# Optimization experiments

Measured on AMD Instinct MI355X. Metric: run time of the kernel, lower is better.

Reference implementation:

```python
import jax, jax.numpy as jnp
import numpy as np

C_DIM, Q_NUM, U_NUM, BATCH = 512, 8000, 20000, 128


def _edges(key, src_lo, src_hi, dst_lo, dst_hi, n_edges):
    k1, k2 = jax.random.split(key)
    src = jax.random.randint(k1, (n_edges,), src_lo, src_hi, dtype=jnp.int32)
    dst = jax.random.randint(k2, (n_edges,), dst_lo, dst_hi, dtype=jnp.int32)
    return jnp.stack([src, dst])


def setup_inputs() -> dict:
    key = jax.random.key(0)
    ks = jax.random.split(key, 20)
    C, Q, U, B = C_DIM, Q_NUM, U_NUM, BATCH
    inv = 1.0 / np.sqrt(C)
    q_tab = (jax.random.uniform(ks[0], (Q, C)) < (4.0 / C)).astype(jnp.float32)
    q_tab = q_tab.at[:, 0].set(1.0)  # ensure every question has >=1 concept
    return {
        'user_id': jax.random.randint(ks[1], (B,), 0, U, dtype=jnp.int32),
        'question_id': jax.random.randint(ks[2], (B,), 0, Q, dtype=jnp.int32),
        'q_table': q_tab,
        'edges_dir': _edges(ks[3], 0, C, 0, C, 4096),
        'edges_und': _edges(ks[4], 0, C, 0, C, 8192),
        'edges_ke': _edges(ks[5], 0, Q, Q, Q + C, 40000),   # exercise -> concept
        'edges_ek': _edges(ks[6], Q, Q + C, 0, Q, 40000),   # concept -> exercise
        'edges_ue': _edges(ks[7], 0, Q, Q, Q + U, 100000),  # exercise -> student
        'edges_eu': _edges(ks[8], Q, Q + U, 0, Q, 100000),  # student -> exercise
        'user_emb': jax.random.normal(ks[9], (U, C)) * inv,
        'question_emb': jax.random.normal(ks[10], (Q, C)) * inv,
        'concept_emb': jax.random.normal(ks[11], (C, C)) * inv,
        'gat_W': jax.random.normal(ks[12], (2, 6, C, C)) * inv,
        'gat_a': jax.random.normal(ks[13], (2, 6, 2 * C)) * inv,
        'attn_w': jax.random.normal(ks[14], (2, 5, 2 * C)) * inv,
        'attn_b': jnp.zeros((2, 5)),
        'W1': jax.random.normal(ks[15], (2 * C, C)) * inv,
        'W2': jax.random.normal(ks[16], (2 * C, C)) * inv,
        'W3': jax.random.normal(ks[17], (C, 1)) * inv,
        'b3': jnp.zeros((1,)),
    }


def gat(h, W, a, src, dst, n_nodes):
    """RCD GraphLayer: linear, per-dst edge softmax of leaky_relu scores, weighted sum."""
    z = h @ W                                   # [N, C]
    zs, zd = z[src], z[dst]                     # [E, C] gathers
    e = jnp.concatenate([zs, zd], axis=1) @ a   # [E]
    e = jnp.where(e > 0, e, 0.01 * e)           # leaky_relu(0.01)
    m = jax.lax.stop_gradient(jax.ops.segment_max(e, dst, num_segments=n_nodes))
    ex = jnp.exp(e - m[dst])
    den = jax.ops.segment_sum(ex, dst, num_segments=n_nodes)
    alpha = ex / den[dst]
    return jax.ops.segment_sum(alpha[:, None] * zs, dst, num_segments=n_nodes)


def fusion(kn, ex, stu, Ws, As, aw, ab, e_dir, e_und, e_ke, e_ek, e_ue, e_eu):
    C, Q, U = kn.shape[0], ex.shape[0], stu.shape[0]
    k_dir = gat(kn, Ws[0], As[0], e_dir[0], e_dir[1], C)
    k_und = gat(kn, Ws[1], As[1], e_und[0], e_und[1], C)
    ekg = jnp.concatenate([ex, kn], axis=0)
    kfe = gat(ekg, Ws[2], As[2], e_ke[0], e_ke[1], Q + C)
    efk = gat(ekg, Ws[3], As[3], e_ek[0], e_ek[1], Q + C)
    eug = jnp.concatenate([ex, stu], axis=0)
    ufe = gat(eug, Ws[4], As[4], e_ue[0], e_ue[1], Q + U)
    efu = gat(eug, Ws[5], As[5], e_eu[0], e_eu[1], Q + U)
    D = kfe[Q:]
    s1 = jnp.concatenate([kn, k_dir], 1) @ aw[0] + ab[0]
    s2 = jnp.concatenate([kn, k_und], 1) @ aw[1] + ab[1]
    s3 = jnp.concatenate([kn, D], 1) @ aw[2] + ab[2]
    s = jax.nn.softmax(jnp.stack([s1, s2, s3], axis=1), axis=1)  # [C, 3]
    kn_out = kn + s[:, 0:1] * k_dir + s[:, 1:2] * k_und + s[:, 2:3] * D
    Bq, Cq = efk[:Q], efu[:Q]
    t1 = jnp.concatenate([ex, Bq], 1) @ aw[3] + ab[3]
    t2 = jnp.concatenate([ex, Cq], 1) @ aw[4] + ab[4]
    t = jax.nn.softmax(jnp.stack([t1, t2], axis=1), axis=1)      # [Q, 2]
    ex_out = ex + t[:, 0:1] * Bq + t[:, 1:2] * Cq
    stu_out = stu + ufe[Q:]
    return kn_out, ex_out, stu_out


def reference(user_id, question_id, q_table, edges_dir, edges_und, edges_ke, edges_ek,
              edges_ue, edges_eu, user_emb, question_emb, concept_emb, gat_W, gat_a,
              attn_w, attn_b, W1, W2, W3, b3):
    C = concept_emb.shape[0]
    kn1, ex1, stu1 = fusion(concept_emb, question_emb, user_emb, gat_W[0], gat_a[0],
                            attn_w[0], attn_b[0], edges_dir, edges_und, edges_ke,
                            edges_ek, edges_ue, edges_eu)
    kn2, ex2, stu2 = fusion(kn1, ex1, stu1, gat_W[1], gat_a[1], attn_w[1], attn_b[1],
                            edges_dir, edges_und, edges_ke, edges_ek, edges_ue, edges_eu)
    sb = stu2[user_id]       # [B, C]
    eb = ex2[question_id]    # [B, C]
    # cat([stu_vector, kn_vector]) @ W1 == stu@W1[:C] (bcast over j) + kn@W1[C:] (bcast over b)
    pref = jax.nn.sigmoid((sb @ W1[:C])[:, None, :] + (kn2 @ W1[C:])[None])  # [B, C, C]
    diff = jax.nn.sigmoid((eb @ W2[:C])[:, None, :] + (kn2 @ W2[C:])[None])  # [B, C, C]
    o = jax.nn.sigmoid((pref - diff) @ W3 + b3)                              # [B, C, 1]
    qb = q_table[question_id]                                                 # [B, C]
    sum_out = jnp.sum(o[..., 0] * qb, axis=1)
    count = jnp.sum(qb, axis=1)
    return sum_out / count
```

## Files before the change

### kernel.cpp

```cpp
#include <hip/hip_runtime.h>
#include <math.h>

#define CD 512
#define CDCD (CD * CD)
#define QN 8000
#define UN 20000
#define BATCHN 128

typedef unsigned short u16;
typedef unsigned int u32;
typedef __attribute__((ext_vector_type(8))) __bf16 bf16x8;
typedef __attribute__((ext_vector_type(4))) float f32x4;

static __device__ __forceinline__ u16 f2bf(float x) {
    u32 u = __float_as_uint(x);
    return (u16)((u + 0x7fff + ((u >> 16) & 1)) >> 16);
}
static __device__ __forceinline__ float bf2f(u16 h) {
    return __uint_as_float(((u32)h) << 16);
}
static __device__ __forceinline__ u32 pck(u16 a, u16 b) {
    return (u32)a | ((u32)b << 16);
}

#define SBM 32
#define SBN 64
#define SBK 32

__global__ __launch_bounds__(256) void gemm_f32_s(
    const float* __restrict__ A, int nfix,
    const int* __restrict__ rowlist, const int* __restrict__ nrow,
    const float* __restrict__ B0, float* __restrict__ C0,
    const float* __restrict__ B1, float* __restrict__ C1)
{
    const int n = nrow ? *nrow : nfix;
    const int bm = blockIdx.x * SBM;
    if (bm >= n) return;
    __shared__ __align__(16) float As[SBM][SBK + 4];
    __shared__ __align__(16) float Bs[SBK][SBN];
    const int which = blockIdx.y >> 3;
    const float* __restrict__ B = which ? B1 : B0;
    float* __restrict__ C = which ? C1 : C0;
    const int bn = (blockIdx.y & 7) * SBN;
    const int tid = threadIdx.x;
    const int ty = tid >> 3, tx = tid & 7;
    const int am = tid >> 3, ak = (tid & 7) * 4;
    const int bk = tid >> 3, bc = (tid & 7) * 8;
    const int gr = bm + am;
    const bool aok = gr < n;
    const int arow = aok ? (rowlist ? rowlist[gr] : gr) : 0;
    const float* Arow = A + (size_t)arow * CD;

    float acc[8];
#pragma unroll
    for (int j = 0; j < 8; j++) acc[j] = 0.f;

    for (int k0 = 0; k0 < CD; k0 += SBK) {
        float4 av = make_float4(0.f, 0.f, 0.f, 0.f);
        if (aok) av = *(const float4*)(Arow + k0 + ak);
        float4 bv0 = *(const float4*)(B + (size_t)(k0 + bk) * CD + bn + bc);
        float4 bv1 = *(const float4*)(B + (size_t)(k0 + bk) * CD + bn + bc + 4);
        __syncthreads();
        *(float4*)&As[am][ak] = av;
        *(float4*)&Bs[bk][bc] = bv0;
        *(float4*)&Bs[bk][bc + 4] = bv1;
        __syncthreads();
#pragma unroll
        for (int kk = 0; kk < SBK; kk++) {
            float a = As[ty][kk];
            float4 b0 = *(const float4*)&Bs[kk][tx * 8];
            float4 b1 = *(const float4*)&Bs[kk][tx * 8 + 4];
            acc[0] = fmaf(a, b0.x, acc[0]); acc[1] = fmaf(a, b0.y, acc[1]);
            acc[2] = fmaf(a, b0.z, acc[2]); acc[3] = fmaf(a, b0.w, acc[3]);
            acc[4] = fmaf(a, b1.x, acc[4]); acc[5] = fmaf(a, b1.y, acc[5]);
            acc[6] = fmaf(a, b1.z, acc[6]); acc[7] = fmaf(a, b1.w, acc[7]);
        }
    }
    if (gr < n) {
        int orow = rowlist ? rowlist[gr] : gr;
        *(float4*)(C + (size_t)orow * CD + bn + tx * 8) =
            make_float4(acc[0], acc[1], acc[2], acc[3]);
        *(float4*)(C + (size_t)orow * CD + bn + tx * 8 + 4) =
            make_float4(acc[4], acc[5], acc[6], acc[7]);
    }
}

__global__ __launch_bounds__(256) void conv_a(
    const float* __restrict__ src, u16* __restrict__ h, u16* __restrict__ l, int n)
{
    const int row = blockIdx.x * 256 + threadIdx.x;
    const int kc = blockIdx.y;
    const int n_pad = gridDim.x * 256;
    float4 v0 = make_float4(0.f, 0.f, 0.f, 0.f), v1 = v0;
    if (row < n) {
        v0 = *(const float4*)(src + (size_t)row * CD + kc * 8);
        v1 = *(const float4*)(src + (size_t)row * CD + kc * 8 + 4);
    }
    float a[8] = {v0.x, v0.y, v0.z, v0.w, v1.x, v1.y, v1.z, v1.w};
    u16 hh[8], ll[8];
#pragma unroll
    for (int e = 0; e < 8; e++) {
        hh[e] = f2bf(a[e]);
        ll[e] = f2bf(a[e] - bf2f(hh[e]));
    }
    size_t o = ((size_t)kc * n_pad + row) * 8;
    uint4 H = make_uint4(pck(hh[0],hh[1]), pck(hh[2],hh[3]), pck(hh[4],hh[5]), pck(hh[6],hh[7]));
    uint4 L = make_uint4(pck(ll[0],ll[1]), pck(ll[2],ll[3]), pck(ll[4],ll[5]), pck(ll[6],ll[7]));
    *(uint4*)(h + o) = H;
    *(uint4*)(l + o) = L;
}

struct WcJobs { const float* src[5]; u16* h[5]; u16* l[5]; };
__global__ __launch_bounds__(256) void conv_bw(WcJobs J)
{
    const int w = blockIdx.z;
    const float* src = J.src[w];
    const int col = blockIdx.x * 256 + threadIdx.x;
    const int kc = blockIdx.y;
    float a[8];
#pragma unroll
    for (int j = 0; j < 8; j++)
        a[j] = src[(size_t)(kc * 8 + j) * CD + col];
    u16 hh[8], ll[8];
#pragma unroll
    for (int e = 0; e < 8; e++) {
        hh[e] = f2bf(a[e]);
        ll[e] = f2bf(a[e] - bf2f(hh[e]));
    }
    size_t o = ((size_t)kc * CD + col) * 8;
    uint4 H = make_uint4(pck(hh[0],hh[1]), pck(hh[2],hh[3]), pck(hh[4],hh[5]), pck(hh[6],hh[7]));
    uint4 L = make_uint4(pck(ll[0],ll[1]), pck(ll[2],ll[3]), pck(ll[4],ll[5]), pck(ll[6],ll[7]));
    *(uint4*)(J.h[w] + o) = H;
    *(uint4*)(J.l[w] + o) = L;
}

__global__ __launch_bounds__(256) void gemm_bf3(
    const u16* __restrict__ Ah, const u16* __restrict__ Al, int n, int n_pad,
    const u16* __restrict__ Bh0, const u16* __restrict__ Bl0, float* __restrict__ C0,
    const u16* __restrict__ Bh1, const u16* __restrict__ Bl1, float* __restrict__ C1)
{
    __shared__ __align__(16) u16 As_h[4][128][8];
    __shared__ __align__(16) u16 As_l[4][128][8];
    __shared__ __align__(16) u16 Bs_h[4][128][8];
    __shared__ __align__(16) u16 Bs_l[4][128][8];
    const int which = blockIdx.y >> 2;
    const u16* Bh = which ? Bh1 : Bh0;
    const u16* Bl = which ? Bl1 : Bl0;
    float* C = which ? C1 : C0;
    const int bm = blockIdx.x * 128, bn = (blockIdx.y & 3) * 128;
    const int tid = threadIdx.x, lane = tid & 63, w = tid >> 6;
    const int wm = w >> 1, wn = w & 1;
    const int l15 = lane & 15, kq = lane >> 4;

    f32x4 acc[4][4];
#pragma unroll
    for (int i = 0; i < 4; i++)
#pragma unroll
        for (int j = 0; j < 4; j++) {
            acc[i][j][0] = 0.f; acc[i][j][1] = 0.f;
            acc[i][j][2] = 0.f; acc[i][j][3] = 0.f;
        }

    for (int kt = 0; kt < 16; ++kt) {
        if (kt) __syncthreads();
#pragma unroll
        for (int s = 0; s < 8; ++s) {
            int ci = tid + s * 256;
            int mat = ci >> 9, rem = ci & 511, kc = rem >> 7, pos = rem & 127;
            int kcg = kt * 4 + kc;
            const u16* g;
            u16* lds;
            if (mat == 0)      { g = Ah + ((size_t)kcg * n_pad + bm + pos) * 8; lds = &As_h[kc][pos][0]; }
            else if (mat == 1) { g = Al + ((size_t)kcg * n_pad + bm + pos) * 8; lds = &As_l[kc][pos][0]; }
            else if (mat == 2) { g = Bh + ((size_t)kcg * CD + bn + pos) * 8;    lds = &Bs_h[kc][pos][0]; }
            else               { g = Bl + ((size_t)kcg * CD + bn + pos) * 8;    lds = &Bs_l[kc][pos][0]; }
            *(uint4*)lds = *(const uint4*)g;
        }
        __syncthreads();
        bf16x8 ah[4], al[4], bh[4], bl[4];
#pragma unroll
        for (int f = 0; f < 4; ++f) {
            ah[f] = *(const bf16x8*)&As_h[kq][wm * 64 + f * 16 + l15][0];
            al[f] = *(const bf16x8*)&As_l[kq][wm * 64 + f * 16 + l15][0];
            bh[f] = *(const bf16x8*)&Bs_h[kq][wn * 64 + f * 16 + l15][0];
            bl[f] = *(const bf16x8*)&Bs_l[kq][wn * 64 + f * 16 + l15][0];
        }
#pragma unroll
        for (int i = 0; i < 4; ++i)
#pragma unroll
            for (int j = 0; j < 4; ++j) {
                acc[i][j] = __builtin_amdgcn_mfma_f32_16x16x32_bf16(ah[i], bh[j], acc[i][j], 0, 0, 0);
                acc[i][j] = __builtin_amdgcn_mfma_f32_16x16x32_bf16(ah[i], bl[j], acc[i][j], 0, 0, 0);
                acc[i][j] = __builtin_amdgcn_mfma_f32_16x16x32_bf16(al[i], bh[j], acc[i][j], 0, 0, 0);
            }
    }
#pragma unroll
    for (int i = 0; i < 4; ++i) {
        int rb = bm + wm * 64 + i * 16 + kq * 4;
#pragma unroll
        for (int j = 0; j < 4; ++j) {
            int col = bn + wn * 64 + j * 16 + l15;
#pragma unroll
            for (int r = 0; r < 4; ++r) {
                int row = rb + r;
                if (row < n) C[(size_t)row * CD + col] = acc[i][j][r];
            }
        }
    }
}

__global__ __launch_bounds__(256) void dot_rows(
    const float* __restrict__ H, const int* __restrict__ sel,
    const float* __restrict__ v, float* __restrict__ out, int n)
{
    const int lane = threadIdx.x & 63;
    const int r = blockIdx.x * 4 + (threadIdx.x >> 6);
    if (r >= n) return;
    const int row = sel ? sel[r] : r;
    const float* h = H + (size_t)row * CD;
    float4 a0 = *(const float4*)(h + lane * 8);
    float4 a1 = *(const float4*)(h + lane * 8 + 4);
    float4 b0 = *(const float4*)(v + lane * 8);
    float4 b1 = *(const float4*)(v + lane * 8 + 4);
    float sv = a0.x * b0.x + a0.y * b0.y + a0.z * b0.z + a0.w * b0.w
             + a1.x * b1.x + a1.y * b1.y + a1.z * b1.z + a1.w * b1.w;
#pragma unroll
    for (int o = 32; o; o >>= 1) sv += __shfl_xor(sv, o, 64);
    if (lane == 0) out[r] = sv;
}

__global__ __launch_bounds__(256) void dot_rows_gather(
    const float* __restrict__ H, const int* __restrict__ rowlist,
    const int* __restrict__ nrow,
    const float* __restrict__ v, float* __restrict__ out)
{
    const int lane = threadIdx.x & 63;
    const int r = blockIdx.x * 4 + (threadIdx.x >> 6);
    if (r >= *nrow) return;
    const int row = rowlist[r];
    const float* h = H + (size_t)row * CD;
    float4 a0 = *(const float4*)(h + lane * 8);
    float4 a1 = *(const float4*)(h + lane * 8 + 4);
    float4 b0 = *(const float4*)(v + lane * 8);
    float4 b1 = *(const float4*)(v + lane * 8 + 4);
    float sv = a0.x * b0.x + a0.y * b0.y + a0.z * b0.z + a0.w * b0.w
             + a1.x * b1.x + a1.y * b1.y + a1.z * b1.z + a1.w * b1.w;
#pragma unroll
    for (int o = 32; o; o >>= 1) sv += __shfl_xor(sv, o, 64);
    if (lane == 0) out[row] = sv;
}

__global__ __launch_bounds__(256) void wa_gemv6(
    const float* __restrict__ W6, const float* __restrict__ a6, float* __restrict__ wa)
{
    const int layer = blockIdx.y;
    const int lane = threadIdx.x & 63;
    const int r = blockIdx.x * 4 + (threadIdx.x >> 6);
    const float* Wr = W6 + (size_t)layer * CDCD + (size_t)r * CD;
    const float* ah = a6 + layer * 2 * CD + CD;
    float4 a0 = *(const float4*)(Wr + lane * 8);
    float4 a1 = *(const float4*)(Wr + lane * 8 + 4);
    float4 b0 = *(const float4*)(ah + lane * 8);
    float4 b1 = *(const float4*)(ah + lane * 8 + 4);
    float sv = a0.x * b0.x + a0.y * b0.y + a0.z * b0.z + a0.w * b0.w
             + a1.x * b1.x + a1.y * b1.y + a1.z * b1.z + a1.w * b1.w;
#pragma unroll
    for (int o = 32; o; o >>= 1) sv += __shfl_xor(sv, o, 64);
    if (lane == 0) wa[layer * CD + r] = sv;
}
// ... 33 lines not shown

    int running = 0;
    for (int base = 0; base < n; base += 1024) {
        int idx = base + tid;
        int v0 = (idx < n) ? cnt[idx] : 0;
        int v = v0;
#pragma unroll
        for (int dlt = 1; dlt < 64; dlt <<= 1) {
            int t = __shfl_up(v, dlt, 64);
            if (lane >= dlt) v += t;
        }
        if (lane == 63) wsum[wid] = v;
        __syncthreads();
        if (wid == 0) {
            int wv = (lane < 16) ? wsum[lane] : 0;
#pragma unroll
            for (int dlt = 1; dlt < 16; dlt <<= 1) {
                int t = __shfl_up(wv, dlt, 64);
                if (lane >= dlt) wv += t;
            }
            if (lane < 16) wsum[lane] = wv;
        }
        __syncthreads();
        int wprefix = (wid > 0) ? wsum[wid - 1] : 0;
        int chunk_total = wsum[15];
        int excl = running + wprefix + (v - v0);
        if (idx < n) { off[idx] = excl; cur[idx] = excl; }
        running += chunk_total;
        __syncthreads();
    }
    if (tid == 0) off[n] = running;
}

__global__ __launch_bounds__(256) void csr_scatter(Csr6 G)
{
    const int total = G.ecum[6];
    for (int idx = blockIdx.x * 256 + threadIdx.x; idx < total; idx += gridDim.x * 256) {
        int g = 0;
        while (idx >= G.ecum[g + 1]) g++;
        int e = idx - G.ecum[g];
        int dl = G.dst[g][e] - G.base[g];
        int pos = atomicAdd(&G.cur[g][dl], 1);
        G.srcs[g][pos] = G.src[g][e];
    }
}

__global__ void mark_qsel(const int* __restrict__ qid, int* __restrict__ qsel)
{
    qsel[qid[threadIdx.x]] = 1;
}

__global__ void mark_user(const int* __restrict__ uid, int* __restrict__ usel,
                          int* __restrict__ umark, int* __restrict__ list,
                          int* __restrict__ nlist)
{
    int u = uid[threadIdx.x];
    usel[u] = 1;
    if (atomicExch(&umark[u], 1) == 0)
        list[atomicAdd(nlist, 1)] = u;
}

__global__ __launch_bounds__(256) void mark_l5(
    const int* __restrict__ esrc, const int* __restrict__ edst, int ne,
    const int* __restrict__ qsel, int* __restrict__ umark,
    int* __restrict__ list, int* __restrict__ nlist)
{
    for (int e = blockIdx.x * 256 + threadIdx.x; e < ne; e += gridDim.x * 256) {
        if (qsel[edst[e]]) {
            int u = esrc[e] - QN;
            if (atomicExch(&umark[u], 1) == 0)
                list[atomicAdd(nlist, 1)] = u;
        }
    }
}

__global__ __launch_bounds__(256) void mark_l4(
    const int* __restrict__ esrc, const int* __restrict__ edst, int ne,
    const int* __restrict__ usel, int* __restrict__ qmark,
    int* __restrict__ qlist, int* __restrict__ nq)
{
    for (int e = blockIdx.x * 256 + threadIdx.x; e < ne; e += gridDim.x * 256) {
        if (usel[edst[e] - QN]) {
            int q = esrc[e];
            if (atomicExch(&qmark[q], 1) == 0)
                qlist[atomicAdd(nq, 1)] = q;
        }
    }
}

__global__ __launch_bounds__(256) void gat_aggregate(
    const int* __restrict__ off, const int* __restrict__ srcs, int src_base,
    const int* __restrict__ sel, const int* __restrict__ nlimit,
    int scatter_out, int dv_node,
    const float* __restrict__ z, const float* __restrict__ s,
    const float* __restrict__ dvals,
    const float* __restrict__ base, float* __restrict__ out)
{
    const int b = blockIdx.x;
    if (nlimit && b >= *nlimit) return;
    const int node = sel ? sel[b] : b;
    const int orow = scatter_out ? node : b;
    const int tid = threadIdx.x;
    const int lane = tid & 63, wid = tid >> 6;
    const int beg = off[node], end = off[node + 1];

    float2 bacc = base ? *(const float2*)(base + (size_t)node * CD + tid * 2)
                       : make_float2(0.f, 0.f);
    if (beg == end) {
        *(float2*)(out + (size_t)orow * CD + tid * 2) = bacc;
        return;
    }
    const float dd = dvals[dv_node ? node : b];

    float m = -1e30f, den = 0.f;
    for (int e = beg + tid; e < end; e += 256) {
        float sc = s[srcs[e] - src_base] + dd;
        sc = sc > 0.f ? sc : 0.01f * sc;
        if (sc > m) { den = den * __expf(m - sc) + 1.f; m = sc; }
        else den += __expf(sc - m);
    }
#pragma unroll
    for (int o = 32; o; o >>= 1) {
        float om = __shfl_xor(m, o, 64);
        float od = __shfl_xor(den, o, 64);
        float nm = fmaxf(m, om);
        den = den * __expf(m - nm) + od * __expf(om - nm);
        m = nm;
    }
    __shared__ float wm[4], wd[4];
    __shared__ float alpha_s[256];
    __shared__ int   src_s[256];
    if (lane == 0) { wm[wid] = m; wd[wid] = den; }
    __syncthreads();
    float M = fmaxf(fmaxf(wm[0], wm[1]), fmaxf(wm[2], wm[3]));
    float Dn = wd[0] * __expf(wm[0] - M) + wd[1] * __expf(wm[1] - M)
             + wd[2] * __expf(wm[2] - M) + wd[3] * __expf(wm[3] - M);
    float invD = 1.f / Dn;

    for (int c0 = beg; c0 < end; c0 += 256) {
        int e = c0 + tid;
        float al = 0.f; int sr = 0;
        if (e < end) {
            sr = srcs[e] - src_base;
            float sc = s[sr] + dd;
            sc = sc > 0.f ? sc : 0.01f * sc;
            al = __expf(sc - M) * invD;
        }
        __syncthreads();
        alpha_s[tid] = al; src_s[tid] = sr;
        __syncthreads();
        int cc = min(256, end - c0);
        for (int jj = 0; jj < cc; jj++) {
            const float* zr = z + (size_t)src_s[jj] * CD;
            float a = alpha_s[jj];
            float2 v = *(const float2*)(zr + tid * 2);
            bacc.x = fmaf(a, v.x, bacc.x);
            bacc.y = fmaf(a, v.y, bacc.y);
        }
    }
    *(float2*)(out + (size_t)orow * CD + tid * 2) = bacc;
}

__global__ __launch_bounds__(256) void fuse_kn(
    const float* __restrict__ kn, const float* __restrict__ kd,
    const float* __restrict__ ku, const float* __restrict__ Dm,
    const float* __restrict__ aw, const float* __restrict__ ab, float* __restrict__ out)
{
    const int i = blockIdx.x, tid = threadIdx.x;
    const int lane = tid & 63, wid = tid >> 6;
    const size_t ro = (size_t)i * CD + tid * 2;
    const int c = tid * 2;
    float2 vkn = *(const float2*)(kn + ro);
    float2 v1  = *(const float2*)(kd + ro);
    float2 v2  = *(const float2*)(ku + ro);
    float2 v3  = *(const float2*)(Dm + ro);
    float p1 = vkn.x*aw[c]      + vkn.y*aw[c+1]      + v1.x*aw[CD+c]      + v1.y*aw[CD+c+1];
    float p2 = vkn.x*aw[1024+c] + vkn.y*aw[1024+c+1] + v2.x*aw[1024+CD+c] + v2.y*aw[1024+CD+c+1];
    float p3 = vkn.x*aw[2048+c] + vkn.y*aw[2048+c+1] + v3.x*aw[2048+CD+c] + v3.y*aw[2048+CD+c+1];
#pragma unroll
    for (int o = 32; o; o >>= 1) {
        p1 += __shfl_xor(p1, o, 64); p2 += __shfl_xor(p2, o, 64); p3 += __shfl_xor(p3, o, 64);
    }
    __shared__ float r1[4], r2[4], r3[4];
    if (lane == 0) { r1[wid] = p1; r2[wid] = p2; r3[wid] = p3; }
    __syncthreads();
    float s1 = r1[0]+r1[1]+r1[2]+r1[3] + ab[0];
    float s2 = r2[0]+r2[1]+r2[2]+r2[3] + ab[1];
    float s3 = r3[0]+r3[1]+r3[2]+r3[3] + ab[2];
    float mm = fmaxf(s1, fmaxf(s2, s3));
    float e1 = __expf(s1-mm), e2 = __expf(s2-mm), e3 = __expf(s3-mm);
    float inv = 1.f / (e1 + e2 + e3);
    float w1 = e1*inv, w2 = e2*inv, w3 = e3*inv;
    float2 o_;
    o_.x = vkn.x + w1*v1.x + w2*v2.x + w3*v3.x;
    o_.y = vkn.y + w1*v1.y + w2*v2.y + w3*v3.y;
    *(float2*)(out + ro) = o_;
// ... 45 lines not shown
    const int tid = threadIdx.x, lane = tid & 63, wid = tid >> 6;
    __shared__ int   sidx[CD];
    __shared__ float sqv[CD];
    __shared__ int   snn;
    __shared__ float scnt[4], sacc[4];
    if (tid == 0) snn = 0;
    __syncthreads();
    const float* qrow = q_table + (size_t)qid[b] * CD;
    float cnt = 0.f;
    for (int i = tid; i < CD; i += 256) {
        float qv = qrow[i];
        if (qv != 0.f) {
            int p = atomicAdd(&snn, 1);
            sidx[p] = i; sqv[p] = qv;
            cnt += qv;
        }
    }
#pragma unroll
    for (int o = 32; o; o >>= 1) cnt += __shfl_xor(cnt, o, 64);
    if (lane == 0) scnt[wid] = cnt;
    __syncthreads();
    const int nn = snn;
    const float bb = b3[0];
    const float* sPr = sP + (size_t)b * CD;
    const float* dPr = dP + (size_t)b * CD;
    float acc = 0.f;
    for (int t = wid; t < nn; t += 4) {
        const int i = sidx[t];
        const float* kPr = kP + (size_t)i * CD;
        const float* kDr = kD + (size_t)i * CD;
        float o = 0.f;
#pragma unroll
        for (int p = 0; p < 8; p++) {
            int j = lane + (p << 6);
            float pv = sPr[j] + kPr[j];
            float dv = dPr[j] + kDr[j];
            float s1 = 1.f / (1.f + __expf(-pv));
            float s2 = 1.f / (1.f + __expf(-dv));
            o += (s1 - s2) * W3[j];
        }
#pragma unroll
        for (int ofs = 32; ofs; ofs >>= 1) o += __shfl_xor(o, ofs, 64);
        if (lane == 0) acc += sqv[t] / (1.f + __expf(-(o + bb)));
    }
    if (lane == 0) sacc[wid] = acc;
    __syncthreads();
    if (tid == 0)
        out[b] = (sacc[0] + sacc[1] + sacc[2] + sacc[3])
               / (scnt[0] + scnt[1] + scnt[2] + scnt[3]);
}

#define EXPAD 8192
#define STUPAD 20224

extern "C" void kernel_launch(void* const* d_in, const int* in_sizes, int n_in,
                              void* d_out, int out_size, void* d_ws, size_t ws_size,
                              hipStream_t stream)
{
    const int*   user_id      = (const int*)d_in[0];
    const int*   question_id  = (const int*)d_in[1];
    const float* q_table      = (const float*)d_in[2];
    const int*   e_dir        = (const int*)d_in[3];
    const int*   e_und        = (const int*)d_in[4];
    const int*   e_ke         = (const int*)d_in[5];
    const int*   e_ek         = (const int*)d_in[6];
    const int*   e_ue         = (const int*)d_in[7];
    const int*   e_eu         = (const int*)d_in[8];
    const float* user_emb     = (const float*)d_in[9];
    const float* question_emb = (const float*)d_in[10];
    const float* concept_emb  = (const float*)d_in[11];
    const float* gat_W        = (const float*)d_in[12];
    const float* gat_a        = (const float*)d_in[13];
    const float* attn_w       = (const float*)d_in[14];
    const float* attn_b       = (const float*)d_in[15];
    const float* W1           = (const float*)d_in[16];
    const float* W2           = (const float*)d_in[17];
    const float* W3           = (const float*)d_in[18];
    const float* b3           = (const float*)d_in[19];
    float* out = (float*)d_out;

    char* wptr = (char*)d_ws;
    auto alloc = [&](size_t bytes) -> void* {
        void* p = (void*)wptr;
        wptr += (bytes + 255) & ~(size_t)255;
        return p;
    };

    float* zone = (float*)alloc((size_t)UN * CD * 4);
    float* z2 = zone;
    float* z4 = zone + (size_t)QN * CD;
    float* z5 = zone;
    float* z0 = (float*)alloc((size_t)CD * CD * 4);
    float* z1 = (float*)alloc((size_t)CD * CD * 4);
    float* z3 = (float*)alloc((size_t)CD * CD * 4);

    float* s0 = (float*)alloc((size_t)CD * 4);
    float* s1 = (float*)alloc((size_t)CD * 4);
    float* s2 = (float*)alloc((size_t)QN * 4);
    float* s3 = (float*)alloc((size_t)CD * 4);
    float* s4 = (float*)alloc((size_t)QN * 4);
    float* s5 = (float*)alloc((size_t)UN * 4);
    float* dv0 = (float*)alloc((size_t)CD * 4);
    float* dv1 = (float*)alloc((size_t)CD * 4);
    float* dv2 = (float*)alloc((size_t)CD * 4);
    float* dv3 = (float*)alloc((size_t)QN * 4);
    float* dv4 = (float*)alloc((size_t)UN * 4);
    float* dv5 = (float*)alloc((size_t)QN * 4);
    float* wa  = (float*)alloc((size_t)6 * CD * 4);

    float* kn1  = (float*)alloc((size_t)CD * CD * 4);
    float* ex1  = (float*)alloc((size_t)QN * CD * 4);
    float* stu1 = (float*)alloc((size_t)UN * CD * 4);
    float* kn2  = (float*)alloc((size_t)CD * CD * 4);
    float* kdir = (float*)alloc((size_t)CD * CD * 4);
    float* kund = (float*)alloc((size_t)CD * CD * 4);
    float* Dm   = (float*)alloc((size_t)CD * CD * 4);
    float* Bq   = (float*)alloc((size_t)QN * CD * 4);
    float* Cq   = (float*)alloc((size_t)QN * CD * 4);
    float* eb   = (float*)alloc((size_t)BATCHN * CD * 4);
    float* sb   = (float*)alloc((size_t)BATCHN * CD * 4);
    float* sP   = (float*)alloc((size_t)BATCHN * CD * 4);
    float* dP   = (float*)alloc((size_t)BATCHN * CD * 4);
    float* kP   = (float*)alloc((size_t)CD * CD * 4);
    float* kD   = (float*)alloc((size_t)CD * CD * 4);

    u16* expH  = (u16*)alloc((size_t)64 * EXPAD * 8 * 2);
    u16* expL  = (u16*)alloc((size_t)64 * EXPAD * 8 * 2);
    u16* stupH = (u16*)alloc((size_t)64 * STUPAD * 8 * 2);
    u16* stupL = (u16*)alloc((size_t)64 * STUPAD * 8 * 2);
    u16* BpH[5]; u16* BpL[5];
    for (int i = 0; i < 5; i++) {
        BpH[i] = (u16*)alloc((size_t)64 * CD * 8 * 2);
        BpL[i] = (u16*)alloc((size_t)64 * CD * 8 * 2);
    }

    static const int g_ne[6]   = {4096, 8192, 40000, 40000, 100000, 100000};
    static const int g_nd[6]   = {512, 512, 512, QN, UN, QN};
    static const int g_base[6] = {0, 0, QN, 0, QN, 0};
    const int* g_edges[6] = {e_dir, e_und, e_ke, e_ek, e_ue, e_eu};

    int cnt_total = 0;
    for (int g = 0; g < 6; g++) cnt_total += g_nd[g];
    int* zbase = (int*)alloc((size_t)(cnt_total + QN + UN + 1 + UN + QN + 1) * 4);
    int* cnt6[6];
    {
        int o = 0;
        for (int g = 0; g < 6; g++) { cnt6[g] = zbase + o; o += g_nd[g]; }
    }
    int* qsel   = zbase + cnt_total;
    int* umark  = qsel + QN;
    int* nlist  = umark + UN;
    int* usel   = nlist + 1;
    int* qmark  = usel + UN;
    int* nq2    = qmark + QN;
    const int ZTOT = cnt_total + QN + UN + 1 + UN + QN + 1;

    int* cur6   = (int*)alloc((size_t)cnt_total * 4);
    int* list   = (int*)alloc((size_t)UN * 4);
    int* qlist2 = (int*)alloc((size_t)QN * 4);
    int* off[6]; int* srcs[6];
    for (int g = 0; g < 6; g++) {
        off[g]  = (int*)alloc((size_t)(g_nd[g] + 1) * 4);
        srcs[g] = (int*)alloc((size_t)g_ne[g] * 4);
    }

    Csr6 G;
    {
        int o = 0, ec = 0;
        for (int g = 0; g < 6; g++) {
            G.src[g] = g_edges[g];
            G.dst[g] = g_edges[g] + g_ne[g];
            G.cnt[g] = cnt6[g];
            G.off[g] = off[g];
            G.cur[g] = cur6 + o;
            G.srcs[g] = srcs[g];
            G.nd[g] = g_nd[g];
            G.base[g] = g_base[g];
            G.ecum[g] = ec;
            o += g_nd[g]; ec += g_ne[g];
        }
        G.ecum[6] = ec;
    }

    zero_ints<<<128, 256, 0, stream>>>(zbase, ZTOT);
    csr_hist<<<512, 256, 0, stream>>>(G);
    csr_scan<<<6, 1024, 0, stream>>>(G);
    csr_scatter<<<512, 256, 0, stream>>>(G);
    mark_qsel<<<1, BATCHN, 0, stream>>>(question_id, qsel);
    mark_user<<<1, BATCHN, 0, stream>>>(user_id, usel, umark, list, nlist);
    mark_l5<<<200, 256, 0, stream>>>(e_eu, e_eu + 100000, 100000, qsel, umark, list, nlist);
    mark_l4<<<200, 256, 0, stream>>>(e_ue, e_ue + 100000, 100000, usel, qmark, qlist2, nq2);

    {
        WcJobs wj;
        const int fl[5][2] = {{0,2},{0,4},{0,5},{1,2},{1,4}};
        for (int i = 0; i < 5; i++) {
            wj.src[i] = gat_W + (size_t)(fl[i][0] * 6 + fl[i][1]) * CDCD;
            wj.h[i] = BpH[i]; wj.l[i] = BpL[i];
        }
        conv_bw<<<dim3(2, 64, 5), 256, 0, stream>>>(wj);
    }

    auto gemm_s = [&](const float* A, int n, const int* rl, const int* nr,
                      const float* B0, float* C0, const float* B1, float* C1, int gx) {
        dim3 g(gx, B1 ? 16 : 8);
        gemm_f32_s<<<g, 256, 0, stream>>>(A, n, rl, nr, B0, C0, B1, C1);
    };
    auto dots = [&](const float* H, const int* sel, const float* v, float* o, int n) {
        dot_rows<<<(n + 3) / 4, 256, 0, stream>>>(H, sel, v, o, n);
    };
    auto agg = [&](int g, int src_base, const int* sel, const int* nlim, int sc, int dvn,
                   const float* z, const float* s, const float* dv,
                   const float* base, float* o, int nblk) {
        gat_aggregate<<<nblk, 256, 0, stream>>>(off[g], srcs[g], src_base, sel, nlim,
                                                sc, dvn, z, s, dv, base, o);
    };

    auto run_fusion = [&](int f, const float* kn, const float* ex, const float* stu,
                          const int* selq, const int* selu,
                          float* kn_o, float* ex_o, float* stu_o) {
        const float* Wf  = gat_W  + (size_t)f * 6 * CDCD;
        const float* af  = gat_a  + (size_t)f * 6 * 2 * CD;
        const float* awf = attn_w + (size_t)f * 5 * 2 * CD;
        const float* abf = attn_b + (size_t)f * 5;
        const int bp = f * 3;

        conv_a<<<dim3(EXPAD / 256, 64), 256, 0, stream>>>(ex, expH, expL, QN);
        if (!selq)
            conv_a<<<dim3(STUPAD / 256, 64), 256, 0, stream>>>(stu, stupH, stupL, UN);

        wa_gemv6<<<dim3(128, 6), 256, 0, stream>>>(Wf, af, wa);

        gemm_s(kn, CD, nullptr, nullptr, Wf + 0 * CDCD, z0, Wf + 1 * CDCD, z1, CD / SBM);
        dots(z0, nullptr, af + 0 * 2 * CD, s0, CD);
        dots(z1, nullptr, af + 1 * 2 * CD, s1, CD);
        dots(kn, nullptr, wa + 0 * CD, dv0, CD);
        dots(kn, nullptr, wa + 1 * CD, dv1, CD);
        agg(0, 0, nullptr, nullptr, 0, 0, z0, s0, dv0, nullptr, kdir, CD);
        agg(1, 0, nullptr, nullptr, 0, 0, z1, s1, dv1, nullptr, kund, CD);

        if (!selq) {
            gemm_bf3<<<dim3((QN + 127) / 128, 8), 256, 0, stream>>>(
                expH, expL, QN, EXPAD,
                BpH[bp + 0], BpL[bp + 0], z2,
                BpH[bp + 1], BpL[bp + 1], z4);
        } else {
            gemm_bf3<<<dim3((QN + 127) / 128, 4), 256, 0, stream>>>(
                expH, expL, QN, EXPAD,
                BpH[bp + 0], BpL[bp + 0], z2,
                nullptr, nullptr, nullptr);
            gemm_s(ex, 0, qlist2, nq2, Wf + 4 * CDCD, z4, nullptr, nullptr, QN / SBM);
        }
        dots(z2, nullptr, af + 2 * 2 * CD, s2, QN);
        dots(kn, nullptr, wa + 2 * CD, dv2, CD);
        agg(2, 0, nullptr, nullptr, 0, 0, z2, s2, dv2, nullptr, Dm, CD);

        gemm_s(kn, CD, nullptr, nullptr, Wf + 3 * CDCD, z3, nullptr, nullptr, CD / SBM);
        dots(z3, nullptr, af + 3 * 2 * CD, s3, CD);
        if (!selq) {
            dots(ex, nullptr, wa + 3 * CD, dv3, QN);
            agg(3, QN, nullptr, nullptr, 0, 0, z3, s3, dv3, nullptr, Bq, QN);
        } else {
            dots(ex, selq, wa + 3 * CD, dv3, BATCHN);
            agg(3, QN, selq, nullptr, 0, 0, z3, s3, dv3, nullptr, Bq, BATCHN);
        }

        if (!selq) {
            dots(z4, nullptr, af + 4 * 2 * CD, s4, QN);
            dot_rows_gather<<<(UN + 3) / 4, 256, 0, stream>>>(stu, list, nlist,
                                                              wa + 4 * CD, dv4);
            agg(4, 0, list, nlist, 1, 1, z4, s4, dv4, stu, stu_o, UN);
        } else {
            dot_rows_gather<<<(QN + 3) / 4, 256, 0, stream>>>(z4, qlist2, nq2,
                                                              af + 4 * 2 * CD, s4);
            dots(stu, selu, wa + 4 * CD, dv4, BATCHN);
            agg(4, 0, selu, nullptr, 0, 0, z4, s4, dv4, stu, stu_o, BATCHN);
        }

        if (!selq) {
            gemm_bf3<<<dim3((UN + 127) / 128, 4), 256, 0, stream>>>(
                stupH, stupL, UN, STUPAD,
                BpH[bp + 2], BpL[bp + 2], z5,
                nullptr, nullptr, nullptr);
            dots(z5, nullptr, af + 5 * 2 * CD, s5, UN);
            dots(ex, nullptr, wa + 5 * CD, dv5, QN);
            agg(5, QN, nullptr, nullptr, 0, 0, z5, s5, dv5, nullptr, Cq, QN);
        } else {
            gemm_s(stu, 0, list, nlist, Wf + 5 * CDCD, z5, nullptr, nullptr, UN / SBM);
            dot_rows_gather<<<(UN + 3) / 4, 256, 0, stream>>>(z5, list, nlist,
                                                              af + 5 * 2 * CD, s5);
            dots(ex, selq, wa + 5 * CD, dv5, BATCHN);
            agg(5, QN, selq, nullptr, 0, 0, z5, s5, dv5, nullptr, Cq, BATCHN);
        }

        fuse_kn<<<CD, 256, 0, stream>>>(kn, kdir, kund, Dm, awf, abf, kn_o);
        fuse_ex<<<selq ? BATCHN : QN, 256, 0, stream>>>(ex, selq, Bq, Cq, awf, abf, ex_o);
    };

    run_fusion(0, concept_emb, question_emb, user_emb, nullptr, nullptr,
               kn1, ex1, stu1);
    run_fusion(1, kn1, ex1, stu1, question_id, user_id,
               kn2, eb, sb);

    gemm_s(sb, BATCHN, nullptr, nullptr, W1, sP, nullptr, nullptr, BATCHN / SBM);
    gemm_s(eb, BATCHN, nullptr, nullptr, W2, dP, nullptr, nullptr, BATCHN / SBM);
    gemm_s(kn2, CD, nullptr, nullptr, W1 + (size_t)CDCD, kP, W2 + (size_t)CDCD, kD, CD / SBM);
    final_pred<<<BATCHN, 256, 0, stream>>>(sP, kP, dP, kD, W3, b3, q_table, question_id, out);
}
```

Before: 880.9 us.

## Replace scalar fp32 SGEMMs with split-bf16 MFMA GEMMs using compacted row lists

Removes the scalar fp32 tiled GEMM and sends every projection, including the kn, sparse-selected ex and stu, and final W1/W2 GEMMs, through the split-bf16 (hi/lo) MFMA GEMM. All 12 GAT weights and the W1/W2 halves are pre-converted once. For the sparse second fusion, selected rows are gathered into a compact converted buffer. A rank map translates source ids to compact positions in the aggregation kernel, and the GEMM exits early past the dynamic row count. This trades extra conversion launches and indirection for using matrix cores instead of FMA loops on the remaining GEMMs.

```diff
diff --git a/kernel.cpp b/kernel.cpp
--- a/kernel.cpp
+++ b/kernel.cpp
@@ -23,76 +23,18 @@
     return (u32)a | ((u32)b << 16);
 }
 
-#define SBM 32
-#define SBN 64
-#define SBK 32
-
-__global__ __launch_bounds__(256) void gemm_f32_s(
-    const float* __restrict__ A, int nfix,
-    const int* __restrict__ rowlist, const int* __restrict__ nrow,
-    const float* __restrict__ B0, float* __restrict__ C0,
-    const float* __restrict__ B1, float* __restrict__ C1)
-{
-    const int n = nrow ? *nrow : nfix;
-    const int bm = blockIdx.x * SBM;
-    if (bm >= n) return;
-    __shared__ __align__(16) float As[SBM][SBK + 4];
-    __shared__ __align__(16) float Bs[SBK][SBN];
-    const int which = blockIdx.y >> 3;
-    const float* __restrict__ B = which ? B1 : B0;
-    float* __restrict__ C = which ? C1 : C0;
-    const int bn = (blockIdx.y & 7) * SBN;
-    const int tid = threadIdx.x;
-    const int ty = tid >> 3, tx = tid & 7;
-    const int am = tid >> 3, ak = (tid & 7) * 4;
-    const int bk = tid >> 3, bc = (tid & 7) * 8;
-    const int gr = bm + am;
-    const bool aok = gr < n;
-    const int arow = aok ? (rowlist ? rowlist[gr] : gr) : 0;
-    const float* Arow = A + (size_t)arow * CD;
-
-    float acc[8];
-#pragma unroll
-    for (int j = 0; j < 8; j++) acc[j] = 0.f;
-
-    for (int k0 = 0; k0 < CD; k0 += SBK) {
-        float4 av = make_float4(0.f, 0.f, 0.f, 0.f);
-        if (aok) av = *(const float4*)(Arow + k0 + ak);
-        float4 bv0 = *(const float4*)(B + (size_t)(k0 + bk) * CD + bn + bc);
-        float4 bv1 = *(const float4*)(B + (size_t)(k0 + bk) * CD + bn + bc + 4);
-        __syncthreads();
-        *(float4*)&As[am][ak] = av;
-        *(float4*)&Bs[bk][bc] = bv0;
-        *(float4*)&Bs[bk][bc + 4] = bv1;
-        __syncthreads();
-#pragma unroll
-        for (int kk = 0; kk < SBK; kk++) {
-            float a = As[ty][kk];
-            float4 b0 = *(const float4*)&Bs[kk][tx * 8];
-            float4 b1 = *(const float4*)&Bs[kk][tx * 8 + 4];
-            acc[0] = fmaf(a, b0.x, acc[0]); acc[1] = fmaf(a, b0.y, acc[1]);
-            acc[2] = fmaf(a, b0.z, acc[2]); acc[3] = fmaf(a, b0.w, acc[3]);
-            acc[4] = fmaf(a, b1.x, acc[4]); acc[5] = fmaf(a, b1.y, acc[5]);
-            acc[6] = fmaf(a, b1.z, acc[6]); acc[7] = fmaf(a, b1.w, acc[7]);
-        }
-    }
-    if (gr < n) {
-        int orow = rowlist ? rowlist[gr] : gr;
-        *(float4*)(C + (size_t)orow * CD + bn + tx * 8) =
-            make_float4(acc[0], acc[1], acc[2], acc[3]);
-        *(float4*)(C + (size_t)orow * CD + bn + tx * 8 + 4) =
-            make_float4(acc[4], acc[5], acc[6], acc[7]);
-    }
-}
-
 __global__ __launch_bounds__(256) void conv_a(
-    const float* __restrict__ src, u16* __restrict__ h, u16* __restrict__ l, int n)
-{
-    const int row = blockIdx.x * 256 + threadIdx.x;
+    const float* __restrict__ src, const int* __restrict__ rowlist,
+    const int* __restrict__ nrow,
+    u16* __restrict__ h, u16* __restrict__ l, int nfix)
+{
+    const int r = blockIdx.x * 256 + threadIdx.x;
     const int kc = blockIdx.y;
     const int n_pad = gridDim.x * 256;
+    const int n = nrow ? *nrow : nfix;
     float4 v0 = make_float4(0.f, 0.f, 0.f, 0.f), v1 = v0;
-    if (row < n) {
+    if (r < n) {
+        const int row = rowlist ? rowlist[r] : r;
         v0 = *(const float4*)(src + (size_t)row * CD + kc * 8);
         v1 = *(const float4*)(src + (size_t)row * CD + kc * 8 + 4);
     }
@@ -103,14 +45,15 @@
         hh[e] = f2bf(a[e]);
         ll[e] = f2bf(a[e] - bf2f(hh[e]));
     }
-    size_t o = ((size_t)kc * n_pad + row) * 8;
+    size_t o = ((size_t)kc * n_pad + r) * 8;
     uint4 H = make_uint4(pck(hh[0],hh[1]), pck(hh[2],hh[3]), pck(hh[4],hh[5]), pck(hh[6],hh[7]));
     uint4 L = make_uint4(pck(ll[0],ll[1]), pck(ll[2],ll[3]), pck(ll[4],ll[5]), pck(ll[6],ll[7]));
     *(uint4*)(h + o) = H;
     *(uint4*)(l + o) = L;
 }
 
-struct WcJobs { const float* src[5]; u16* h[5]; u16* l[5]; };
+#define NWC 16
+struct WcJobs { const float* src[NWC]; u16* h[NWC]; u16* l[NWC]; };
 __global__ __launch_bounds__(256) void conv_bw(WcJobs J)
 {
     const int w = blockIdx.z;
@@ -135,10 +78,14 @@
 }
 
 __global__ __launch_bounds__(256) void gemm_bf3(
-    const u16* __restrict__ Ah, const u16* __restrict__ Al, int n, int n_pad,
+    const u16* __restrict__ Ah, const u16* __restrict__ Al, int nfix,
+    const int* __restrict__ nrow, int n_pad,
     const u16* __restrict__ Bh0, const u16* __restrict__ Bl0, float* __restrict__ C0,
     const u16* __restrict__ Bh1, const u16* __restrict__ Bl1, float* __restrict__ C1)
 {
+    const int n = nrow ? *nrow : nfix;
+    const int bm = blockIdx.x * 128;
+    if (bm >= n) return;
     __shared__ __align__(16) u16 As_h[4][128][8];
     __shared__ __align__(16) u16 As_l[4][128][8];
     __shared__ __align__(16) u16 Bs_h[4][128][8];
@@ -147,7 +94,7 @@
     const u16* Bh = which ? Bh1 : Bh0;
     const u16* Bl = which ? Bl1 : Bl0;
     float* C = which ? C1 : C0;
-    const int bm = blockIdx.x * 128, bn = (blockIdx.y & 3) * 128;
+    const int bn = (blockIdx.y & 3) * 128;
     const int tid = threadIdx.x, lane = tid & 63, w = tid >> 6;
     const int wm = w >> 1, wn = w & 1;
     const int l15 = lane & 15, kq = lane >> 4;
@@ -211,10 +158,12 @@
 
 __global__ __launch_bounds__(256) void dot_rows(
     const float* __restrict__ H, const int* __restrict__ sel,
-    const float* __restrict__ v, float* __restrict__ out, int n)
+    const float* __restrict__ v, float* __restrict__ out, int nfix,
+    const int* __restrict__ nrow)
 {
     const int lane = threadIdx.x & 63;
     const int r = blockIdx.x * 4 + (threadIdx.x >> 6);
+    const int n = nrow ? *nrow : nfix;
     if (r >= n) return;
     const int row = sel ? sel[r] : r;
     const float* h = H + (size_t)row * CD;
@@ -354,24 +303,30 @@
 
 __global__ void mark_user(const int* __restrict__ uid, int* __restrict__ usel,
                           int* __restrict__ umark, int* __restrict__ list,
-                          int* __restrict__ nlist)
+                          int* __restrict__ nlist, int* __restrict__ rank5)
 {
     int u = uid[threadIdx.x];
     usel[u] = 1;
-    if (atomicExch(&umark[u], 1) == 0)
-        list[atomicAdd(nlist, 1)] = u;
+    if (atomicExch(&umark[u], 1) == 0) {
+        int p = atomicAdd(nlist, 1);
+        list[p] = u;
+        rank5[u] = p;
+    }
 }
 
 __global__ __launch_bounds__(256) void mark_l5(
     const int* __restrict__ esrc, const int* __restrict__ edst, int ne,
     const int* __restrict__ qsel, int* __restrict__ umark,
-    int* __restrict__ list, int* __restrict__ nlist)
+    int* __restrict__ list, int* __restrict__ nlist, int* __restrict__ rank5)
 {
     for (int e = blockIdx.x * 256 + threadIdx.x; e < ne; e += gridDim.x * 256) {
         if (qsel[edst[e]]) {
             int u = esrc[e] - QN;
-            if (atomicExch(&umark[u], 1) == 0)
-                list[atomicAdd(nlist, 1)] = u;
+            if (atomicExch(&umark[u], 1) == 0) {
+                int p = atomicAdd(nlist, 1);
+                list[p] = u;
+                rank5[u] = p;
+            }
         }
     }
 }
@@ -379,19 +334,23 @@
 __global__ __launch_bounds__(256) void mark_l4(
     const int* __restrict__ esrc, const int* __restrict__ edst, int ne,
     const int* __restrict__ usel, int* __restrict__ qmark,
-    int* __restrict__ qlist, int* __restrict__ nq)
+    int* __restrict__ qlist, int* __restrict__ nq, int* __restrict__ rank4)
 {
     for (int e = blockIdx.x * 256 + threadIdx.x; e < ne; e += gridDim.x * 256) {
         if (usel[edst[e] - QN]) {
             int q = esrc[e];
-            if (atomicExch(&qmark[q], 1) == 0)
-                qlist[atomicAdd(nq, 1)] = q;
+            if (atomicExch(&qmark[q], 1) == 0) {
+                int p = atomicAdd(nq, 1);
+                qlist[p] = q;
+                rank4[q] = p;
+            }
         }
     }
 }
 
 __global__ __launch_bounds__(256) void gat_aggregate(
     const int* __restrict__ off, const int* __restrict__ srcs, int src_base,
+    const int* __restrict__ rank,
     const int* __restrict__ sel, const int* __restrict__ nlimit,
     int scatter_out, int dv_node,
     const float* __restrict__ z, const float* __restrict__ s,
@@ -416,7 +375,9 @@
 
     float m = -1e30f, den = 0.f;
     for (int e = beg + tid; e < end; e += 256) {
-        float sc = s[srcs[e] - src_base] + dd;
+        int sr = srcs[e] - src_base;
+        if (rank) sr = rank[sr];
+        float sc = s[sr] + dd;
         sc = sc > 0.f ? sc : 0.01f * sc;
         if (sc > m) { den = den * __expf(m - sc) + 1.f; m = sc; }
         else den += __expf(sc - m);
@@ -444,6 +405,7 @@
         float al = 0.f; int sr = 0;
         if (e < end) {
             sr = srcs[e] - src_base;
+            if (rank) sr = rank[sr];
             float sc = s[sr] + dd;
             sc = sc > 0.f ? sc : 0.01f * sc;
             al = __expf(sc - M) * invD;
@@ -595,6 +557,7 @@
 
 #define EXPAD 8192
 #define STUPAD 20224
+#define SMPAD 256
 
 extern "C" void kernel_launch(void* const* d_in, const int* in_sizes, int n_in,
                               void* d_out, int out_size, void* d_ws, size_t ws_size,
@@ -667,12 +630,16 @@
     float* kP   = (float*)alloc((size_t)CD * CD * 4);
     float* kD   = (float*)alloc((size_t)CD * CD * 4);
 
-    u16* expH  = (u16*)alloc((size_t)64 * EXPAD * 8 * 2);
-    u16* expL  = (u16*)alloc((size_t)64 * EXPAD * 8 * 2);
-    u16* stupH = (u16*)alloc((size_t)64 * STUPAD * 8 * 2);
-    u16* stupL = (u16*)alloc((size_t)64 * STUPAD * 8 * 2);
-    u16* BpH[5]; u16* BpL[5];
-    for (int i = 0; i < 5; i++) {
+    u16* exH  = (u16*)alloc((size_t)64 * EXPAD * 8 * 2);
+    u16* exL  = (u16*)alloc((size_t)64 * EXPAD * 8 * 2);
+    u16* stuH = (u16*)alloc((size_t)64 * STUPAD * 8 * 2);
+    u16* stuL = (u16*)alloc((size_t)64 * STUPAD * 8 * 2);
+    u16* knH  = (u16*)alloc((size_t)64 * CD * 8 * 2);
+    u16* knL  = (u16*)alloc((size_t)64 * CD * 8 * 2);
+    u16* cH   = (u16*)alloc((size_t)64 * EXPAD * 8 * 2);
+    u16* cL   = (u16*)alloc((size_t)64 * EXPAD * 8 * 2);
+    u16* BpH[NWC]; u16* BpL[NWC];
+    for (int i = 0; i < NWC; i++) {
         BpH[i] = (u16*)alloc((size_t)64 * CD * 8 * 2);
         BpL[i] = (u16*)alloc((size_t)64 * CD * 8 * 2);
     }
@@ -701,6 +668,8 @@
     int* cur6   = (int*)alloc((size_t)cnt_total * 4);
     int* list   = (int*)alloc((size_t)UN * 4);
     int* qlist2 = (int*)alloc((size_t)QN * 4);
+    int* rank5  = (int*)alloc((size_t)UN * 4);
+    int* rank4  = (int*)alloc((size_t)QN * 4);
     int* off[6]; int* srcs[6];
     for (int g = 0; g < 6; g++) {
         off[g]  = (int*)alloc((size_t)(g_nd[g] + 1) * 4);
@@ -730,110 +699,115 @@
     csr_scan<<<6, 1024, 0, stream>>>(G);
     csr_scatter<<<512, 256, 0, stream>>>(G);
     mark_qsel<<<1, BATCHN, 0, stream>>>(question_id, qsel);
-    mark_user<<<1, BATCHN, 0, stream>>>(user_id, usel, umark, list, nlist);
-    mark_l5<<<200, 256, 0, stream>>>(e_eu, e_eu + 100000, 100000, qsel, umark, list, nlist);
-    mark_l4<<<200, 256, 0, stream>>>(e_ue, e_ue + 100000, 100000, usel, qmark, qlist2, nq2);
+    mark_user<<<1, BATCHN, 0, stream>>>(user_id, usel, umark, list, nlist, rank5);
+    mark_l5<<<200, 256, 0, stream>>>(e_eu, e_eu + 100000, 100000, qsel, umark,
+                                     list, nlist, rank5);
+    mark_l4<<<200, 256, 0, stream>>>(e_ue, e_ue + 100000, 100000, usel, qmark,
+                                     qlist2, nq2, rank4);
 
     {
         WcJobs wj;
-        const int fl[5][2] = {{0,2},{0,4},{0,5},{1,2},{1,4}};
-        for (int i = 0; i < 5; i++) {
-            wj.src[i] = gat_W + (size_t)(fl[i][0] * 6 + fl[i][1]) * CDCD;
-            wj.h[i] = BpH[i]; wj.l[i] = BpL[i];
-        }
-        conv_bw<<<dim3(2, 64, 5), 256, 0, stream>>>(wj);
-    }
-
-    auto gemm_s = [&](const float* A, int n, const int* rl, const int* nr,
-                      const float* B0, float* C0, const float* B1, float* C1, int gx) {
-        dim3 g(gx, B1 ? 16 : 8);
-        gemm_f32_s<<<g, 256, 0, stream>>>(A, n, rl, nr, B0, C0, B1, C1);
+        for (int f = 0; f < 2; f++)
+            for (int l = 0; l < 6; l++)
+                wj.src[f * 6 + l] = gat_W + (size_t)(f * 6 + l) * CDCD;
+        wj.src[12] = W1;
+        wj.src[13] = W1 + (size_t)CDCD;
+        wj.src[14] = W2;
+        wj.src[15] = W2 + (size_t)CDCD;
+        for (int i = 0; i < NWC; i++) { wj.h[i] = BpH[i]; wj.l[i] = BpL[i]; }
+        conv_bw<<<dim3(2, 64, NWC), 256, 0, stream>>>(wj);
+    }
+
+    auto conv = [&](const float* src, const int* rl, const int* nr,
+                    u16* h, u16* l, int nfix, int npad) {
+        conv_a<<<dim3(npad / 256, 64), 256, 0, stream>>>(src, rl, nr, h, l, nfix);
     };
-    auto dots = [&](const float* H, const int* sel, const float* v, float* o, int n) {
-        dot_rows<<<(n + 3) / 4, 256, 0, stream>>>(H, sel, v, o, n);
+    auto bf3 = [&](const u16* Ah, const u16* Al, int nfix, const int* nr, int npad,
+                   int b0, float* C0, int b1, float* C1) {
+        dim3 g((nfix + 127) / 128, (b1 >= 0) ? 8 : 4);
+        gemm_bf3<<<g, 256, 0, stream>>>(Ah, Al, nfix, nr, npad,
+                                        BpH[b0], BpL[b0], C0,
+                                        (b1 >= 0) ? BpH[b1] : nullptr,
+                                        (b1 >= 0) ? BpL[b1] : nullptr, C1);
     };
-    auto agg = [&](int g, int src_base, const int* sel, const int* nlim, int sc, int dvn,
+    auto dots = [&](const float* H, const int* sel, const float* v, float* o,
+                    int n, const int* nr) {
+        dot_rows<<<(n + 3) / 4, 256, 0, stream>>>(H, sel, v, o, n, nr);
+    };
+    auto agg = [&](int g, int src_base, const int* rank, const int* sel,
+                   const int* nlim, int sc, int dvn,
                    const float* z, const float* s, const float* dv,
                    const float* base, float* o, int nblk) {
-        gat_aggregate<<<nblk, 256, 0, stream>>>(off[g], srcs[g], src_base, sel, nlim,
-                                                sc, dvn, z, s, dv, base, o);
+        gat_aggregate<<<nblk, 256, 0, stream>>>(off[g], srcs[g], src_base, rank,
+                                                sel, nlim, sc, dvn, z, s, dv, base, o);
     };
 
     auto run_fusion = [&](int f, const float* kn, const float* ex, const float* stu,
                           const int* selq, const int* selu,
                           float* kn_o, float* ex_o, float* stu_o) {
-        const float* Wf  = gat_W  + (size_t)f * 6 * CDCD;
         const float* af  = gat_a  + (size_t)f * 6 * 2 * CD;
         const float* awf = attn_w + (size_t)f * 5 * 2 * CD;
         const float* abf = attn_b + (size_t)f * 5;
-        const int bp = f * 3;
-
-        conv_a<<<dim3(EXPAD / 256, 64), 256, 0, stream>>>(ex, expH, expL, QN);
-        if (!selq)
-            conv_a<<<dim3(STUPAD / 256, 64), 256, 0, stream>>>(stu, stupH, stupL, UN);
+        const float* Wf  = gat_W  + (size_t)f * 6 * CDCD;
+        const int bp = f * 6;
+
+        conv(ex, nullptr, nullptr, exH, exL, QN, EXPAD);
+        if (!selq) conv(stu, nullptr, nullptr, stuH, stuL, UN, STUPAD);
+        conv(kn, nullptr, nullptr, knH, knL, CD, CD);
 
         wa_gemv6<<<dim3(128, 6), 256, 0, stream>>>(Wf, af, wa);
 
-        gemm_s(kn, CD, nullptr, nullptr, Wf + 0 * CDCD, z0, Wf + 1 * CDCD, z1, CD / SBM);
-        dots(z0, nullptr, af + 0 * 2 * CD, s0, CD);
-        dots(z1, nullptr, af + 1 * 2 * CD, s1, CD);
-        dots(kn, nullptr, wa + 0 * CD, dv0, CD);
-        dots(kn, nullptr, wa + 1 * CD, dv1, CD);
-        agg(0, 0, nullptr, nullptr, 0, 0, z0, s0, dv0, nullptr, kdir, CD);
-        agg(1, 0, nullptr, nullptr, 0, 0, z1, s1, dv1, nullptr, kund, CD);
+        bf3(knH, knL, CD, nullptr, CD, bp + 0, z0, bp + 1, z1);
+        dots(z0, nullptr, af + 0 * 2 * CD, s0, CD, nullptr);
+        dots(z1, nullptr, af + 1 * 2 * CD, s1, CD, nullptr);
+        dots(kn, nullptr, wa + 0 * CD, dv0, CD, nullptr);
+        dots(kn, nullptr, wa + 1 * CD, dv1, CD, nullptr);
+        agg(0, 0, nullptr, nullptr, nullptr, 0, 0, z0, s0, dv0, nullptr, kdir, CD);
+        agg(1, 0, nullptr, nullptr, nullptr, 0, 0, z1, s1, dv1, nullptr, kund, CD);
 
         if (!selq) {
-            gemm_bf3<<<dim3((QN + 127) / 128, 8), 256, 0, stream>>>(
-                expH, expL, QN, EXPAD,
-                BpH[bp + 0], BpL[bp + 0], z2,
-                BpH[bp + 1], BpL[bp + 1], z4);
+            bf3(exH, exL, QN, nullptr, EXPAD, bp + 2, z2, bp + 4, z4);
         } else {
-            gemm_bf3<<<dim3((QN + 127) / 128, 4), 256, 0, stream>>>(
-                expH, expL, QN, EXPAD,
-                BpH[bp + 0], BpL[bp + 0], z2,
-                nullptr, nullptr, nullptr);
-            gemm_s(ex, 0, qlist2, nq2, Wf + 4 * CDCD, z4, nullptr, nullptr, QN / SBM);
-        }
-        dots(z2, nullptr, af + 2 * 2 * CD, s2, QN);
-        dots(kn, nullptr, wa + 2 * CD, dv2, CD);
-        agg(2, 0, nullptr, nullptr, 0, 0, z2, s2, dv2, nullptr, Dm, CD);
-
-        gemm_s(kn, CD, nullptr, nullptr, Wf + 3 * CDCD, z3, nullptr, nullptr, CD / SBM);
-        dots(z3, nullptr, af + 3 * 2 * CD, s3, CD);
+            bf3(exH, exL, QN, nullptr, EXPAD, bp + 2, z2, -1, nullptr);
+        }
+        dots(z2, nullptr, af + 2 * 2 * CD, s2, QN, nullptr);
+        dots(kn, nullptr, wa + 2 * CD, dv2, CD, nullptr);
+        agg(2, 0, nullptr, nullptr, nullptr, 0, 0, z2, s2, dv2, nullptr, Dm, CD);
+
         if (!selq) {
-            dots(ex, nullptr, wa + 3 * CD, dv3, QN);
-            agg(3, QN, nullptr, nullptr, 0, 0, z3, s3, dv3, nullptr, Bq, QN);
-        } else {
-            dots(ex, selq, wa + 3 * CD, dv3, BATCHN);
-            agg(3, QN, selq, nullptr, 0, 0, z3, s3, dv3, nullptr, Bq, BATCHN);
-        }
-
-        if (!selq) {
-            dots(z4, nullptr, af + 4 * 2 * CD, s4, QN);
+            dots(z4, nullptr, af + 4 * 2 * CD, s4, QN, nullptr);
             dot_rows_gather<<<(UN + 3) / 4, 256, 0, stream>>>(stu, list, nlist,
                                                               wa + 4 * CD, dv4);
-            agg(4, 0, list, nlist, 1, 1, z4, s4, dv4, stu, stu_o, UN);
+            agg(4, 0, nullptr, list, nlist, 1, 1, z4, s4, dv4, stu, stu_o, UN);
         } else {
-            dot_rows_gather<<<(QN + 3) / 4, 256, 0, stream>>>(z4, qlist2, nq2,
-                                                              af + 4 * 2 * CD, s4);
-            dots(stu, selu, wa + 4 * CD, dv4, BATCHN);
-            agg(4, 0, selu, nullptr, 0, 0, z4, s4, dv4, stu, stu_o, BATCHN);
-        }
-
+            conv(ex, qlist2, nq2, cH, cL, QN, EXPAD);
+            bf3(cH, cL, QN, nq2, EXPAD, bp + 4, z4, -1, nullptr);
+            dots(z4, nullptr, af + 4 * 2 * CD, s4, QN, nq2);
+            dots(stu, selu, wa + 4 * CD, dv4, BATCHN, nullptr);
+            agg(4, 0, rank4, selu, nullptr, 0, 0, z4, s4, dv4, stu, stu_o, BATCHN);
+        }
+
+        bf3(knH, knL, CD, nullptr, CD, bp + 3, z3, -1, nullptr);
+        dots(z3, nullptr, af + 3 * 2 * CD, s3, CD, nullptr);
         if (!selq) {
-            gemm_bf3<<<dim3((UN + 127) / 128, 4), 256, 0, stream>>>(
-                stupH, stupL, UN, STUPAD,
-                BpH[bp + 2], BpL[bp + 2], z5,
-                nullptr, nullptr, nullptr);
-            dots(z5, nullptr, af + 5 * 2 * CD, s5, UN);
-            dots(ex, nullptr, wa + 5 * CD, dv5, QN);
-            agg(5, QN, nullptr, nullptr, 0, 0, z5, s5, dv5, nullptr, Cq, QN);
+            dots(ex, nullptr, wa + 3 * CD, dv3, QN, nullptr);
+            agg(3, QN, nullptr, nullptr, nullptr, 0, 0, z3, s3, dv3, nullptr, Bq, QN);
         } else {
-            gemm_s(stu, 0, list, nlist, Wf + 5 * CDCD, z5, nullptr, nullptr, UN / SBM);
-            dot_rows_gather<<<(UN + 3) / 4, 256, 0, stream>>>(z5, list, nlist,
-                                                              af + 5 * 2 * CD, s5);
-            dots(ex, selq, wa + 5 * CD, dv5, BATCHN);
-            agg(5, QN, selq, nullptr, 0, 0, z5, s5, dv5, nullptr, Cq, BATCHN);
+            dots(ex, selq, wa + 3 * CD, dv3, BATCHN, nullptr);
+            agg(3, QN, nullptr, selq, nullptr, 0, 0, z3, s3, dv3, nullptr, Bq, BATCHN);
+        }
+
+        if (!selq) {
+            bf3(stuH, stuL, UN, nullptr, STUPAD, bp + 5, z5, -1, nullptr);
+            dots(z5, nullptr, af + 5 * 2 * CD, s5, UN, nullptr);
+            dots(ex, nullptr, wa + 5 * CD, dv5, QN, nullptr);
+            agg(5, QN, nullptr, nullptr, nullptr, 0, 0, z5, s5, dv5, nullptr, Cq, QN);
+        } else {
+            conv(stu, list, nlist, stuH, stuL, UN, STUPAD);
+            bf3(stuH, stuL, UN, nlist, STUPAD, bp + 5, z5, -1, nullptr);
+            dots(z5, nullptr, af + 5 * 2 * CD, s5, UN, nlist);
+            dots(ex, selq, wa + 5 * CD, dv5, BATCHN, nullptr);
+            agg(5, QN, rank5, selq, nullptr, 0, 0, z5, s5, dv5, nullptr, Cq, BATCHN);
         }
 
         fuse_kn<<<CD, 256, 0, stream>>>(kn, kdir, kund, Dm, awf, abf, kn_o);
@@ -845,8 +819,11 @@
     run_fusion(1, kn1, ex1, stu1, question_id, user_id,
                kn2, eb, sb);
 
-    gemm_s(sb, BATCHN, nullptr, nullptr, W1, sP, nullptr, nullptr, BATCHN / SBM);
-    gemm_s(eb, BATCHN, nullptr, nullptr, W2, dP, nullptr, nullptr, BATCHN / SBM);
-    gemm_s(kn2, CD, nullptr, nullptr, W1 + (size_t)CDCD, kP, W2 + (size_t)CDCD, kD, CD / SBM);
+    conv(sb, nullptr, nullptr, cH, cL, BATCHN, SMPAD);
+    bf3(cH, cL, BATCHN, nullptr, SMPAD, 12, sP, -1, nullptr);
+    conv(eb, nullptr, nullptr, cH, cL, BATCHN, SMPAD);
+    bf3(cH, cL, BATCHN, nullptr, SMPAD, 14, dP, -1, nullptr);
+    conv(kn2, nullptr, nullptr, knH, knL, CD, CD);
+    bf3(knH, knL, CD, nullptr, CD, 13, kP, 15, kD);
     final_pred<<<BATCHN, 256, 0, stream>>>(sP, kP, dP, kD, W3, b3, q_table, question_id, out);
 }
```

Measured after the change: 972.5 us. 1.1x slower.
